# Performance work log

Hardware: AMD Instinct MI355X
Metric: run time of the kernel (lower is better)

The kernel has to match this reference:

```python
import jax, jax.numpy as jnp
import numpy as np

ALPHA = 0.2          # LeakyReLU negative slope
NEG_BIG = -9e15      # mask value from original code


def setup_inputs() -> dict:
    key = jax.random.key(0)
    k1, k2, k3, k4 = jax.random.split(key, 4)
    B, N, F_in, F_out = 16, 1024, 256, 256
    x = jax.random.normal(k1, (B, N, F_in), dtype=jnp.float32)
    adj = jax.random.randint(k2, (B, N, N), 0, 2, dtype=jnp.int32)
    # xavier-uniform-like scales
    W = jax.random.normal(k3, (F_in, F_out), dtype=jnp.float32) * np.sqrt(2.0 / (F_in + F_out))
    a = jax.random.normal(k4, (2 * F_out, 1), dtype=jnp.float32) * np.sqrt(2.0 / (2 * F_out + 1))
    return {"x": x, "adj": adj, "W": W, "a": a}


def reference(x, adj, W, a):
    # x: [B,N,Fin], adj: [B,N,N] (int mask), W: [Fin,Fout], a: [2*Fout,1]
    F_out = a.shape[0] // 2
    h = jnp.einsum("bni,io->bno", x, W)            # [B,N,Fout]
    # Decompose a into left/right halves: e_ij = lrelu(a_l.h_i + a_r.h_j)
    a_l = a[:F_out, 0]                               # [Fout]
    a_r = a[F_out:, 0]                               # [Fout]
    el = h @ a_l                                     # [B,N] score contribution of target i
    er = h @ a_r                                     # [B,N] score contribution of source j
    e = jax.nn.leaky_relu(el[:, :, None] + er[:, None, :], ALPHA)  # [B,N,N]
    e = jnp.where(adj > 0, e, NEG_BIG)
    attn = jax.nn.softmax(e, axis=-1)                # masked softmax over neighbors j
    # weighted sum of neighbor features; concat with n_heads=1 is identity
    return jnp.einsum("bij,bjo->bio", attn, h)       # [B,N,Fout]
```

## Files before the change

### kernel.cpp

```cpp
#include <hip/hip_runtime.h>
#include <stdint.h>

#define ALPHA 0.2f
#define NEG_BIG -9000000000000000.0f
#define L2E 1.4426950408889634f

typedef __attribute__((ext_vector_type(8))) short bf16x8;
typedef __attribute__((ext_vector_type(8))) unsigned short u16x8;
typedef __attribute__((ext_vector_type(4))) float f32x4;

__device__ __forceinline__ unsigned short f2bf(float f) {
    unsigned int u = __float_as_uint(f);
    u += 0x7fffu + ((u >> 16) & 1u);
    return (unsigned short)(u >> 16);
}

__device__ __forceinline__ void gload_lds16(const void* g, void* l) {
    __builtin_amdgcn_global_load_lds(
        (const __attribute__((address_space(1))) unsigned int*)g,
        (__attribute__((address_space(3))) unsigned int*)l, 16, 0, 0);
}

__global__ void wt_wa_kernel(const float* __restrict__ W,
                             const float* __restrict__ a,
                             unsigned short* __restrict__ Wtbf,
                             float* __restrict__ wa) {
    const int t = threadIdx.x;
    if (blockIdx.x < 256) {
        const int o = blockIdx.x;
        Wtbf[o * 256 + t] = f2bf(W[t * 256 + o]);
    } else {
        float sl = 0.f, sr = 0.f;
        const float* wr = W + t * 256;
        for (int o = 0; o < 256; ++o) {
            const float wv = wr[o];
            sl += wv * a[o];
            sr += wv * a[256 + o];
        }
        wa[t] = sl;
        wa[256 + t] = sr;
    }
}

__global__ __launch_bounds__(256) void eler2x_kernel(
    const float* __restrict__ x, const float* __restrict__ wa,
    float* __restrict__ el, float* __restrict__ er,
    unsigned short* __restrict__ xbf)
{
    const int w = threadIdx.x >> 6, l = threadIdx.x & 63;
    const int r = blockIdx.x * 4 + w;
    const float4 xv = *(const float4*)(x + (size_t)r * 256 + l * 4);
    const float4 al = *(const float4*)(wa + l * 4);
    const float4 ar = *(const float4*)(wa + 256 + l * 4);

    ushort4 xb;
    xb.x = f2bf(xv.x); xb.y = f2bf(xv.y); xb.z = f2bf(xv.z); xb.w = f2bf(xv.w);
    *(ushort4*)(xbf + (size_t)r * 256 + l * 4) = xb;

    float sl = xv.x * al.x + xv.y * al.y + xv.z * al.z + xv.w * al.w;
    float sr = xv.x * ar.x + xv.y * ar.y + xv.z * ar.z + xv.w * ar.w;
#pragma unroll
    for (int off = 32; off >= 1; off >>= 1) {
        sl += __shfl_xor(sl, off);
        sr += __shfl_xor(sr, off);
    }
    if (l == 0) { el[r] = sl * L2E; er[r] = sr * L2E; }
}

__global__ __launch_bounds__(256) void gemm_h(
    const unsigned short* __restrict__ A,
    const unsigned short* __restrict__ Bt,
    unsigned short* __restrict__ C)
{
    __shared__ __align__(16) unsigned short As[2 * 64 * 64];
    __shared__ __align__(16) unsigned short Bs[2 * 128 * 64];

    const int tid = threadIdx.x;
    const int w = tid >> 6, l = tid & 63;
    const int q = l >> 4, ml = l & 15;
    const int wm = (w >> 1) * 32;
    const int wn = (w & 1) * 64;
    const int m0 = blockIdx.y * 64;
    const int n0 = blockIdx.x * 128;

    f32x4 acc[2][4];
#pragma unroll
    for (int i = 0; i < 2; ++i)
#pragma unroll
        for (int j = 0; j < 4; ++j) {
            f32x4 z = {0.f, 0.f, 0.f, 0.f};
            acc[i][j] = z;
        }

#define GSTAGE(BI, K0) do {                                                   \
    _Pragma("unroll")                                                         \
    for (int c_ = 0; c_ < 2; ++c_) {                                          \
        const int cb_ = c_ * 256 + (w << 6);                                  \
        const int p_ = cb_ + l;                                               \
        const int r_ = p_ >> 3;                                               \
        const int cc_ = (p_ & 7) ^ (r_ & 7);                                  \
        gload_lds16(A + (size_t)(m0 + r_) * 256 + (K0) + cc_ * 8,             \
                    As + (BI) * 4096 + cb_ * 8);                              \
    }                                                                         \
    _Pragma("unroll")                                                         \
    for (int c_ = 0; c_ < 4; ++c_) {                                          \
        const int cb_ = c_ * 256 + (w << 6);                                  \
        const int p_ = cb_ + l;                                               \
        const int r_ = p_ >> 3;                                               \
        const int cc_ = (p_ & 7) ^ (r_ & 7);                                  \
        gload_lds16(Bt + (size_t)(n0 + r_) * 256 + (K0) + cc_ * 8,            \
                    Bs + (BI) * 8192 + cb_ * 8);                              \
    } } while (0)

    GSTAGE(0, 0);

    for (int s = 0; s < 4; ++s) {
        const int cur = s & 1;
        if (s + 1 < 4) {
            GSTAGE((s + 1) & 1, (s + 1) * 64);
            asm volatile("s_waitcnt vmcnt(6) lgkmcnt(0)" ::: "memory");
        } else {
            asm volatile("s_waitcnt vmcnt(0) lgkmcnt(0)" ::: "memory");
        }
        __builtin_amdgcn_s_barrier();
        __builtin_amdgcn_sched_barrier(0);

        const unsigned short* Ab = As + cur * 4096;
        const unsigned short* Bb = Bs + cur * 8192;
        bf16x8 aF[2][2], bF[2][4];
#pragma unroll
        for (int ks = 0; ks < 2; ++ks) {
#pragma unroll
            for (int mt = 0; mt < 2; ++mt) {
                const int mm = wm + mt * 16 + ml;
                aF[ks][mt] = *(const bf16x8*)(Ab + (mm * 8 + ((ks * 4 + q) ^ (mm & 7))) * 8);
            }
#pragma unroll
            for (int nt = 0; nt < 4; ++nt) {
                const int nn = wn + nt * 16 + ml;
                bF[ks][nt] = *(const bf16x8*)(Bb + (nn * 8 + ((ks * 4 + q) ^ (nn & 7))) * 8);
            }
        }
#pragma unroll
        for (int ks = 0; ks < 2; ++ks)
            for (int mt = 0; mt < 2; ++mt)
                for (int nt = 0; nt < 4; ++nt)
                    acc[mt][nt] = __builtin_amdgcn_mfma_f32_16x16x32_bf16(
                        aF[ks][mt], bF[ks][nt], acc[mt][nt], 0, 0, 0);

        asm volatile("s_waitcnt lgkmcnt(0)" ::: "memory");
        __builtin_amdgcn_s_barrier();
    }
#undef GSTAGE

    for (int mt = 0; mt < 2; ++mt)
        for (int nt = 0; nt < 4; ++nt) {
            const int gn = n0 + wn + nt * 16 + ml;
            for (int r = 0; r < 4; ++r) {
                const int gm = m0 + wm + mt * 16 + q * 4 + r;
                C[(size_t)gm * 16384 + gn] = f2bf(acc[mt][nt][r]);
            }
        }
}

__global__ __launch_bounds__(512) void maskpv_kernel(
    const int* __restrict__ adj,
    const float* __restrict__ el2,
    const float* __restrict__ er2,
    const unsigned short* __restrict__ hT,
    float* __restrict__ out)
{
    __shared__ float er_s[1024];
    __shared__ float s_s[32];
    __shared__ __align__(16) unsigned short Hs[2 * 256 * 64];
    __shared__ __align__(16) unsigned short Ps[2 * 32 * 72];

    const int tid = threadIdx.x;
    const int w = tid >> 6, l = tid & 63;
    const int q = l >> 4, ml = l & 15;
    const int wm = (w >> 2) * 16;
    const int wn = (w & 3) * 64;

    const int bid = blockIdx.x;
    const int slot = bid >> 3;
    const int b = ((bid & 7) << 1) | (slot >> 5);
    const int i0 = (slot & 31) * 32;

    const int ib = tid >> 4;
    const int js = (tid & 15) * 4;
    const int rg = (b << 10) + i0 + ib;
    const float el2i = el2[rg];

    const unsigned short* hb = hT + (size_t)b * 1024;

#define STAGE(BI, T) do {                                                     \
    const int jb_ = (T) * 64;                                                 \
    _Pragma("unroll")                                                         \
    for (int c_ = 0; c_ < 4; ++c_) {                                          \
        const int cb_ = c_ * 512 + tid;                                       \
        const int r_ = cb_ >> 3;                                              \
        const int cc_ = (cb_ & 7) ^ (r_ & 7);                                 \
        gload_lds16(hb + (size_t)r_ * 16384 + jb_ + cc_ * 8,                  \
                    Hs + (BI) * 16384 + (cb_ << 3));                          \
    } } while (0)

    STAGE(0, 0);

    *(float2*)(er_s + tid * 2) = *(const float2*)(er2 + (b << 10) + tid * 2);

    const int* arow = adj + (size_t)rg * 1024;
    unsigned mw0 = 0, mw1 = 0;
    {
        int4 av[8];
#pragma unroll
        for (int i = 0; i < 8; ++i)
            av[i] = *(const int4*)(arow + i * 64 + js);
#pragma unroll
        for (int i = 0; i < 8; ++i) {
            const unsigned bits =
                (av[i].x > 0 ? 1u : 0u) | (av[i].y > 0 ? 2u : 0u) |
                (av[i].z > 0 ? 4u : 0u) | (av[i].w > 0 ? 8u : 0u);
            mw0 |= bits << (i * 4);
        }
#pragma unroll
        for (int i = 0; i < 8; ++i)
            av[i] = *(const int4*)(arow + (i + 8) * 64 + js);
#pragma unroll
        for (int i = 0; i < 8; ++i) {
            const unsigned bits =
                (av[i].x > 0 ? 1u : 0u) | (av[i].y > 0 ? 2u : 0u) |
                (av[i].z > 0 ? 4u : 0u) | (av[i].w > 0 ? 8u : 0u);
            mw1 |= bits << (i * 4);
        }
    }

    asm volatile("s_waitcnt lgkmcnt(0)" ::: "memory");
    __builtin_amdgcn_s_barrier();

    f32x4 acc[4];
#pragma unroll
    for (int j = 0; j < 4; ++j) {
        f32x4 z = {0.f, 0.f, 0.f, 0.f};
        acc[j] = z;
    }
    float s0 = 0.f, s1 = 0.f, s2 = 0.f, s3 = 0.f;

#define BUILDR(BI, T) do {                                                    \
    const float4 ev_ = *(const float4*)(er_s + (T) * 64 + js);                \
    const unsigned mv_ =                                                      \
        (((T) < 8) ? (mw0 >> ((T) * 4)) : (mw1 >> (((T) - 8) * 4))) & 0xFu;   \
    float e0_ = el2i + ev_.x; e0_ = fmaxf(e0_, ALPHA * e0_);                  \
    float e1_ = el2i + ev_.y; e1_ = fmaxf(e1_, ALPHA * e1_);                  \
    float e2_ = el2i + ev_.z; e2_ = fmaxf(e2_, ALPHA * e2_);                  \
    float e3_ = el2i + ev_.w; e3_ = fmaxf(e3_, ALPHA * e3_);                  \
    ushort4 pv_;                                                              \
    pv_.x = (mv_ & 1u) ? f2bf(exp2f(e0_)) : (unsigned short)0;                \
    pv_.y = (mv_ & 2u) ? f2bf(exp2f(e1_)) : (unsigned short)0;                \
    pv_.z = (mv_ & 4u) ? f2bf(exp2f(e2_)) : (unsigned short)0;                \
    pv_.w = (mv_ & 8u) ? f2bf(exp2f(e3_)) : (unsigned short)0;                \
    s0 += __uint_as_float((unsigned)pv_.x << 16);                             \
    s1 += __uint_as_float((unsigned)pv_.y << 16);                             \
    s2 += __uint_as_float((unsigned)pv_.z << 16);                             \
    s3 += __uint_as_float((unsigned)pv_.w << 16);                             \
    *(ushort4*)(Ps + (BI) * 2304 + ib * 72 + js) = pv_;                       \
    } while (0)

#define COMPUTE(BI) do {                                                      \
    bf16x8 aF_[2], bF_[2][4];                                                 \
    _Pragma("unroll")                                                         \
    for (int ks_ = 0; ks_ < 2; ++ks_)                                         \
        aF_[ks_] = *(const bf16x8*)(Ps + (BI) * 2304 +                        \
                                    (wm + ml) * 72 + ks_ * 32 + q * 8);       \
    _Pragma("unroll")                                                         \
    for (int ks_ = 0; ks_ < 2; ++ks_)                                         \
        _Pragma("unroll")                                                     \
        for (int nt_ = 0; nt_ < 4; ++nt_) {                                   \
            const int oc_ = wn + nt_ * 16 + ml;                               \
            const int sl_ = (ks_ * 4 + q) ^ (oc_ & 7);                        \
            bF_[ks_][nt_] = *(const bf16x8*)(Hs + (BI) * 16384 +              \
                                             oc_ * 64 + sl_ * 8);             \
        }                                                                     \
    __builtin_amdgcn_s_setprio(1);                                            \
    _Pragma("unroll")                                                         \
    for (int ks_ = 0; ks_ < 2; ++ks_)                                         \
        _Pragma("unroll")                                                     \
        for (int nt_ = 0; nt_ < 4; ++nt_)                                     \
            acc[nt_] = __builtin_amdgcn_mfma_f32_16x16x32_bf16(               \
                aF_[ks_], bF_[ks_][nt_], acc[nt_], 0, 0, 0);                  \
    __builtin_amdgcn_s_setprio(0);                                            \
    } while (0)

#pragma unroll
    for (int t = 0; t < 16; ++t) {
        const int cur = t & 1;
        if (t + 1 < 16) STAGE((t + 1) & 1, t + 1);
        BUILDR(cur, t);
        if (t + 1 < 16)
            asm volatile("s_waitcnt vmcnt(4) lgkmcnt(0)" ::: "memory");
        else
            asm volatile("s_waitcnt vmcnt(0) lgkmcnt(0)" ::: "memory");
        __builtin_amdgcn_s_barrier();
        __builtin_amdgcn_sched_barrier(0);
        COMPUTE(cur);
        asm volatile("s_waitcnt lgkmcnt(0)" ::: "memory");
        __builtin_amdgcn_s_barrier();
    }

#undef STAGE
#undef BUILDR
#undef COMPUTE

    float ssum = (s0 + s1) + (s2 + s3);
#pragma unroll
    for (int off = 1; off <= 8; off <<= 1) ssum += __shfl_xor(ssum, off);
    if ((tid & 15) == 0) s_s[ib] = ssum;
    __syncthreads();

    float* ob = out + (size_t)b * 262144;
    float rinv[4];
#pragma unroll
    for (int r = 0; r < 4; ++r) rinv[r] = 1.0f / s_s[wm + q * 4 + r];
#pragma unroll
    for (int nt = 0; nt < 4; ++nt) {
        const int gn = wn + nt * 16 + ml;
#pragma unroll
        for (int r = 0; r < 4; ++r) {
            const int gm = i0 + wm + q * 4 + r;
            ob[(size_t)gm * 256 + gn] = acc[nt][r] * rinv[r];
        }
    }
}

extern "C" void kernel_launch(void* const* d_in, const int* in_sizes, int n_in,
                              void* d_out, int out_size, void* d_ws, size_t ws_size,
                              hipStream_t stream) {
    const float* x   = (const float*)d_in[0];
    const int*   adj = (const int*)d_in[1];
    const float* W   = (const float*)d_in[2];
    const float* a   = (const float*)d_in[3];
    float* out = (float*)d_out;

    char* ws = (char*)d_ws;
    unsigned short* Wtbf  = (unsigned short*)(ws);
    float* wa             = (float*)(ws + 131072);
    unsigned short* xbf   = (unsigned short*)(ws + 133120);
    unsigned short* h_T   = (unsigned short*)(ws + 8521728);
    float* el             = (float*)(ws + 16910336);
    float* er             = (float*)(ws + 16975872);

    wt_wa_kernel<<<dim3(257), dim3(256), 0, stream>>>(W, a, Wtbf, wa);

    eler2x_kernel<<<dim3(4096), dim3(256), 0, stream>>>(x, wa, el, er, xbf);

    gemm_h<<<dim3(128, 4), dim3(256), 0, stream>>>(Wtbf, xbf, h_T);

    maskpv_kernel<<<dim3(512), dim3(512), 0, stream>>>(adj, el, er, h_T, out);
}
```

Measured before the change: 159.8 us.

## Load H operands directly into registers instead of staging through LDS

The maskpv kernel no longer stages hT tiles into shared memory with global_load_lds. Each wave now loads its B fragments straight from global memory into registers, double-buffered across two register sets, and the loop is restructured into a two-step pipeline that alternates building P with MFMA compute. Launch bounds now request 4 blocks per CU. This removes the LDS footprint for H and the LDS read traffic, allowing higher occupancy. In exchange, the global loads are less coalesced (16 bytes per lane at 32 KB row strides), there is more register pressure, and the barrier count per step goes up.

```diff
diff --git a/kernel.cpp b/kernel.cpp
--- a/kernel.cpp
+++ b/kernel.cpp
@@ -2,11 +2,9 @@
 #include <stdint.h>
 
 #define ALPHA 0.2f
-#define NEG_BIG -9000000000000000.0f
 #define L2E 1.4426950408889634f
 
 typedef __attribute__((ext_vector_type(8))) short bf16x8;
-typedef __attribute__((ext_vector_type(8))) unsigned short u16x8;
 typedef __attribute__((ext_vector_type(4))) float f32x4;
 
 __device__ __forceinline__ unsigned short f2bf(float f) {
@@ -19,6 +17,11 @@
     __builtin_amdgcn_global_load_lds(
         (const __attribute__((address_space(1))) unsigned int*)g,
         (__attribute__((address_space(3))) unsigned int*)l, 16, 0, 0);
+}
+
+__device__ __forceinline__ void bar_lds() {
+    asm volatile("s_waitcnt lgkmcnt(0)" ::: "memory");
+    __builtin_amdgcn_s_barrier();
 }
 
 __global__ void wt_wa_kernel(const float* __restrict__ W,
@@ -163,7 +166,7 @@
         }
 }
 
-__global__ __launch_bounds__(512) void maskpv_kernel(
+__global__ __launch_bounds__(512, 4) void maskpv_kernel(
     const int* __restrict__ adj,
     const float* __restrict__ el2,
     const float* __restrict__ er2,
@@ -172,7 +175,6 @@
 {
     __shared__ float er_s[1024];
     __shared__ float s_s[32];
-    __shared__ __align__(16) unsigned short Hs[2 * 256 * 64];
     __shared__ __align__(16) unsigned short Ps[2 * 32 * 72];
 
     const int tid = threadIdx.x;
@@ -193,18 +195,21 @@
 
     const unsigned short* hb = hT + (size_t)b * 1024;
 
-#define STAGE(BI, T) do {                                                     \
-    const int jb_ = (T) * 64;                                                 \
-    _Pragma("unroll")                                                         \
-    for (int c_ = 0; c_ < 4; ++c_) {                                          \
-        const int cb_ = c_ * 512 + tid;                                       \
-        const int r_ = cb_ >> 3;                                              \
-        const int cc_ = (cb_ & 7) ^ (r_ & 7);                                 \
-        gload_lds16(hb + (size_t)r_ * 16384 + jb_ + cc_ * 8,                  \
-                    Hs + (BI) * 16384 + (cb_ << 3));                          \
+    const unsigned short* bp[4];
+#pragma unroll
+    for (int nt = 0; nt < 4; ++nt)
+        bp[nt] = hb + (size_t)(wn + nt * 16 + ml) * 16384 + q * 8;
+
+    bf16x8 BA[8], BB[8];
+
+#define LOADB(B, T) do {                                                      \
+    _Pragma("unroll")                                                         \
+    for (int nt_ = 0; nt_ < 4; ++nt_) {                                       \
+        B[nt_]     = *(const bf16x8*)(bp[nt_] + (T) * 64);                    \
+        B[4 + nt_] = *(const bf16x8*)(bp[nt_] + (T) * 64 + 32);               \
     } } while (0)
 
-    STAGE(0, 0);
+    LOADB(BA, 0);
 
     *(float2*)(er_s + tid * 2) = *(const float2*)(er2 + (b << 10) + tid * 2);
 
@@ -234,8 +239,7 @@
         }
     }
 
-    asm volatile("s_waitcnt lgkmcnt(0)" ::: "memory");
-    __builtin_amdgcn_s_barrier();
+    bar_lds();
 
     f32x4 acc[4];
 #pragma unroll
@@ -245,7 +249,7 @@
     }
     float s0 = 0.f, s1 = 0.f, s2 = 0.f, s3 = 0.f;
 
-#define BUILDR(BI, T) do {                                                    \
+#define BUILDP(BI, T) do {                                                    \
     const float4 ev_ = *(const float4*)(er_s + (T) * 64 + js);                \
     const unsigned mv_ =                                                      \
         (((T) < 8) ? (mw0 >> ((T) * 4)) : (mw1 >> (((T) - 8) * 4))) & 0xFu;   \
@@ -265,49 +269,41 @@
     *(ushort4*)(Ps + (BI) * 2304 + ib * 72 + js) = pv_;                       \
     } while (0)
 
-#define COMPUTE(BI) do {                                                      \
-    bf16x8 aF_[2], bF_[2][4];                                                 \
+#define COMPUTE(BI, B) do {                                                   \
+    bf16x8 aF_[2];                                                            \
     _Pragma("unroll")                                                         \
     for (int ks_ = 0; ks_ < 2; ++ks_)                                         \
         aF_[ks_] = *(const bf16x8*)(Ps + (BI) * 2304 +                        \
                                     (wm + ml) * 72 + ks_ * 32 + q * 8);       \
-    _Pragma("unroll")                                                         \
-    for (int ks_ = 0; ks_ < 2; ++ks_)                                         \
-        _Pragma("unroll")                                                     \
-        for (int nt_ = 0; nt_ < 4; ++nt_) {                                   \
-            const int oc_ = wn + nt_ * 16 + ml;                               \
-            const int sl_ = (ks_ * 4 + q) ^ (oc_ & 7);                        \
-            bF_[ks_][nt_] = *(const bf16x8*)(Hs + (BI) * 16384 +              \
-                                             oc_ * 64 + sl_ * 8);             \
-        }                                                                     \
     __builtin_amdgcn_s_setprio(1);                                            \
     _Pragma("unroll")                                                         \
     for (int ks_ = 0; ks_ < 2; ++ks_)                                         \
         _Pragma("unroll")                                                     \
         for (int nt_ = 0; nt_ < 4; ++nt_)                                     \
             acc[nt_] = __builtin_amdgcn_mfma_f32_16x16x32_bf16(               \
-                aF_[ks_], bF_[ks_][nt_], acc[nt_], 0, 0, 0);                  \
+                aF_[ks_], B[ks_ * 4 + nt_], acc[nt_], 0, 0, 0);               \
     __builtin_amdgcn_s_setprio(0);                                            \
     } while (0)
 
-#pragma unroll
-    for (int t = 0; t < 16; ++t) {
-        const int cur = t & 1;
-        if (t + 1 < 16) STAGE((t + 1) & 1, t + 1);
-        BUILDR(cur, t);
-        if (t + 1 < 16)
-            asm volatile("s_waitcnt vmcnt(4) lgkmcnt(0)" ::: "memory");
-        else
-            asm volatile("s_waitcnt vmcnt(0) lgkmcnt(0)" ::: "memory");
-        __builtin_amdgcn_s_barrier();
-        __builtin_amdgcn_sched_barrier(0);
-        COMPUTE(cur);
-        asm volatile("s_waitcnt lgkmcnt(0)" ::: "memory");
-        __builtin_amdgcn_s_barrier();
-    }
-
-#undef STAGE
-#undef BUILDR
+    BUILDP(0, 0);
+
+    for (int t = 0; t < 16; t += 2) {
+        LOADB(BB, t + 1);
+        BUILDP(1, t + 1);
+        bar_lds();
+        COMPUTE(0, BA);
+        bar_lds();
+        if (t + 2 < 16) {
+            LOADB(BA, t + 2);
+            BUILDP(0, t + 2);
+        }
+        bar_lds();
+        COMPUTE(1, BB);
+        bar_lds();
+    }
+
+#undef LOADB
+#undef BUILDP
 #undef COMPUTE
 
     float ssum = (s0 + s1) + (s2 + s3);
```

Result: slower. 216.8 us (+35.6%).

## Split masked attention-PV kernel across output-column halves with smaller j tiles

Applied to the files above, without the earlier changes.

The attention/PV kernel now launches 1024 blocks of 256 threads, each covering 32 rows and half of the 256 output features, instead of 512 blocks of 512 threads covering all features. The j dimension is processed in 32-wide steps instead of 64, with smaller LDS buffers and a matching swizzle, which raises block count and occupancy. The cost is that each output half recomputes the exp/mask probabilities and rereads the adjacency rows, doubling adj traffic (the largest input), and the loop has more barriers per unit of work.

```diff
diff --git a/kernel.cpp b/kernel.cpp
--- a/kernel.cpp
+++ b/kernel.cpp
@@ -2,11 +2,9 @@
 #include <stdint.h>
 
 #define ALPHA 0.2f
-#define NEG_BIG -9000000000000000.0f
 #define L2E 1.4426950408889634f
 
 typedef __attribute__((ext_vector_type(8))) short bf16x8;
-typedef __attribute__((ext_vector_type(8))) unsigned short u16x8;
 typedef __attribute__((ext_vector_type(4))) float f32x4;
 
 __device__ __forceinline__ unsigned short f2bf(float f) {
@@ -163,7 +161,7 @@
         }
 }
 
-__global__ __launch_bounds__(512) void maskpv_kernel(
+__global__ __launch_bounds__(256) void maskpv_kernel(
     const int* __restrict__ adj,
     const float* __restrict__ el2,
     const float* __restrict__ er2,
@@ -172,66 +170,61 @@
 {
     __shared__ float er_s[1024];
     __shared__ float s_s[32];
-    __shared__ __align__(16) unsigned short Hs[2 * 256 * 64];
-    __shared__ __align__(16) unsigned short Ps[2 * 32 * 72];
+    __shared__ __align__(16) unsigned short Hs[2 * 128 * 32];
+    __shared__ __align__(16) unsigned short Ps[2 * 32 * 40];
 
     const int tid = threadIdx.x;
     const int w = tid >> 6, l = tid & 63;
     const int q = l >> 4, ml = l & 15;
-    const int wm = (w >> 2) * 16;
-    const int wn = (w & 3) * 64;
+    const int wm = (w >> 1) * 16;
+    const int wn = (w & 1) * 64;
 
     const int bid = blockIdx.x;
     const int slot = bid >> 3;
-    const int b = ((bid & 7) << 1) | (slot >> 5);
-    const int i0 = (slot & 31) * 32;
-
-    const int ib = tid >> 4;
-    const int js = (tid & 15) * 4;
+    const int b = ((bid & 7) << 1) | (slot >> 6);
+    const int rem = slot & 63;
+    const int i0 = (rem >> 1) * 32;
+    const int oh = rem & 1;
+
+    const int ib = tid >> 3;
+    const int js = (tid & 7) * 4;
     const int rg = (b << 10) + i0 + ib;
     const float el2i = el2[rg];
 
-    const unsigned short* hb = hT + (size_t)b * 1024;
+    const unsigned short* hb = hT + (size_t)b * 1024 + (size_t)oh * 128 * 16384;
 
 #define STAGE(BI, T) do {                                                     \
-    const int jb_ = (T) * 64;                                                 \
-    _Pragma("unroll")                                                         \
-    for (int c_ = 0; c_ < 4; ++c_) {                                          \
-        const int cb_ = c_ * 512 + tid;                                       \
-        const int r_ = cb_ >> 3;                                              \
-        const int cc_ = (cb_ & 7) ^ (r_ & 7);                                 \
+    const int jb_ = (T) * 32;                                                 \
+    _Pragma("unroll")                                                         \
+    for (int c_ = 0; c_ < 2; ++c_) {                                          \
+        const int cb_ = c_ * 256 + tid;                                       \
+        const int r_ = cb_ >> 2;                                              \
+        const int cc_ = (cb_ & 3) ^ ((r_ >> 1) & 3);                          \
         gload_lds16(hb + (size_t)r_ * 16384 + jb_ + cc_ * 8,                  \
-                    Hs + (BI) * 16384 + (cb_ << 3));                          \
+                    Hs + (BI) * 4096 + (cb_ << 3));                           \
     } } while (0)
 
     STAGE(0, 0);
 
-    *(float2*)(er_s + tid * 2) = *(const float2*)(er2 + (b << 10) + tid * 2);
-
-    const int* arow = adj + (size_t)rg * 1024;
-    unsigned mw0 = 0, mw1 = 0;
-    {
+    *(float4*)(er_s + tid * 4) = *(const float4*)(er2 + (b << 10) + tid * 4);
+
+    const int* arow = adj + (size_t)rg * 1024 + js;
+    unsigned mw[4] = {0u, 0u, 0u, 0u};
+#pragma unroll
+    for (int bt = 0; bt < 4; ++bt) {
         int4 av[8];
 #pragma unroll
         for (int i = 0; i < 8; ++i)
-            av[i] = *(const int4*)(arow + i * 64 + js);
+            av[i] = *(const int4*)(arow + (bt * 8 + i) * 32);
+        unsigned acc_bits = 0;
 #pragma unroll
         for (int i = 0; i < 8; ++i) {
             const unsigned bits =
                 (av[i].x > 0 ? 1u : 0u) | (av[i].y > 0 ? 2u : 0u) |
                 (av[i].z > 0 ? 4u : 0u) | (av[i].w > 0 ? 8u : 0u);
-            mw0 |= bits << (i * 4);
-        }
-#pragma unroll
-        for (int i = 0; i < 8; ++i)
-            av[i] = *(const int4*)(arow + (i + 8) * 64 + js);
-#pragma unroll
-        for (int i = 0; i < 8; ++i) {
-            const unsigned bits =
-                (av[i].x > 0 ? 1u : 0u) | (av[i].y > 0 ? 2u : 0u) |
-                (av[i].z > 0 ? 4u : 0u) | (av[i].w > 0 ? 8u : 0u);
-            mw1 |= bits << (i * 4);
-        }
+            acc_bits |= bits << (i * 4);
+        }
+        mw[bt] = acc_bits;
     }
 
     asm volatile("s_waitcnt lgkmcnt(0)" ::: "memory");
@@ -246,9 +239,8 @@
     float s0 = 0.f, s1 = 0.f, s2 = 0.f, s3 = 0.f;
 
 #define BUILDR(BI, T) do {                                                    \
-    const float4 ev_ = *(const float4*)(er_s + (T) * 64 + js);                \
-    const unsigned mv_ =                                                      \
-        (((T) < 8) ? (mw0 >> ((T) * 4)) : (mw1 >> (((T) - 8) * 4))) & 0xFu;   \
+    const float4 ev_ = *(const float4*)(er_s + (T) * 32 + js);                \
+    const unsigned mv_ = (mw[(T) >> 3] >> (((T) & 7) * 4)) & 0xFu;            \
     float e0_ = el2i + ev_.x; e0_ = fmaxf(e0_, ALPHA * e0_);                  \
     float e1_ = el2i + ev_.y; e1_ = fmaxf(e1_, ALPHA * e1_);                  \
     float e2_ = el2i + ev_.z; e2_ = fmaxf(e2_, ALPHA * e2_);                  \
@@ -262,41 +254,34 @@
     s1 += __uint_as_float((unsigned)pv_.y << 16);                             \
     s2 += __uint_as_float((unsigned)pv_.z << 16);                             \
     s3 += __uint_as_float((unsigned)pv_.w << 16);                             \
-    *(ushort4*)(Ps + (BI) * 2304 + ib * 72 + js) = pv_;                       \
+    *(ushort4*)(Ps + (BI) * 1280 + ib * 40 + js) = pv_;                       \
     } while (0)
 
 #define COMPUTE(BI) do {                                                      \
-    bf16x8 aF_[2], bF_[2][4];                                                 \
-    _Pragma("unroll")                                                         \
-    for (int ks_ = 0; ks_ < 2; ++ks_)                                         \
-        aF_[ks_] = *(const bf16x8*)(Ps + (BI) * 2304 +                        \
-                                    (wm + ml) * 72 + ks_ * 32 + q * 8);       \
-    _Pragma("unroll")                                                         \
-    for (int ks_ = 0; ks_ < 2; ++ks_)                                         \
-        _Pragma("unroll")                                                     \
-        for (int nt_ = 0; nt_ < 4; ++nt_) {                                   \
-            const int oc_ = wn + nt_ * 16 + ml;                               \
-            const int sl_ = (ks_ * 4 + q) ^ (oc_ & 7);                        \
-            bF_[ks_][nt_] = *(const bf16x8*)(Hs + (BI) * 16384 +              \
-                                             oc_ * 64 + sl_ * 8);             \
-        }                                                                     \
+    const bf16x8 aF_ = *(const bf16x8*)(Ps + (BI) * 1280 +                    \
+                                        (wm + ml) * 40 + q * 8);              \
+    bf16x8 bF_[4];                                                            \
+    _Pragma("unroll")                                                         \
+    for (int nt_ = 0; nt_ < 4; ++nt_) {                                       \
+        const int oc_ = wn + nt_ * 16 + ml;                                   \
+        const int sl_ = q ^ ((oc_ >> 1) & 3);                                 \
+        bF_[nt_] = *(const bf16x8*)(Hs + (BI) * 4096 + oc_ * 32 + sl_ * 8);   \
+    }                                                                         \
     __builtin_amdgcn_s_setprio(1);                                            \
     _Pragma("unroll")                                                         \
-    for (int ks_ = 0; ks_ < 2; ++ks_)                                         \
-        _Pragma("unroll")                                                     \
-        for (int nt_ = 0; nt_ < 4; ++nt_)                                     \
-            acc[nt_] = __builtin_amdgcn_mfma_f32_16x16x32_bf16(               \
-                aF_[ks_], bF_[ks_][nt_], acc[nt_], 0, 0, 0);                  \
+    for (int nt_ = 0; nt_ < 4; ++nt_)                                         \
+        acc[nt_] = __builtin_amdgcn_mfma_f32_16x16x32_bf16(                   \
+            aF_, bF_[nt_], acc[nt_], 0, 0, 0);                                \
     __builtin_amdgcn_s_setprio(0);                                            \
     } while (0)
 
 #pragma unroll
-    for (int t = 0; t < 16; ++t) {
+    for (int t = 0; t < 32; ++t) {
         const int cur = t & 1;
-        if (t + 1 < 16) STAGE((t + 1) & 1, t + 1);
+        if (t + 1 < 32) STAGE((t + 1) & 1, t + 1);
         BUILDR(cur, t);
-        if (t + 1 < 16)
-            asm volatile("s_waitcnt vmcnt(4) lgkmcnt(0)" ::: "memory");
+        if (t + 1 < 32)
+            asm volatile("s_waitcnt vmcnt(2) lgkmcnt(0)" ::: "memory");
         else
             asm volatile("s_waitcnt vmcnt(0) lgkmcnt(0)" ::: "memory");
         __builtin_amdgcn_s_barrier();
@@ -312,11 +297,11 @@
 
     float ssum = (s0 + s1) + (s2 + s3);
 #pragma unroll
-    for (int off = 1; off <= 8; off <<= 1) ssum += __shfl_xor(ssum, off);
-    if ((tid & 15) == 0) s_s[ib] = ssum;
+    for (int off = 1; off <= 4; off <<= 1) ssum += __shfl_xor(ssum, off);
+    if ((tid & 7) == 0) s_s[ib] = ssum;
     __syncthreads();
 
-    float* ob = out + (size_t)b * 262144;
+    float* ob = out + (size_t)b * 262144 + oh * 128;
     float rinv[4];
 #pragma unroll
     for (int r = 0; r < 4; ++r) rinv[r] = 1.0f / s_s[wm + q * 4 + r];
@@ -354,5 +339,5 @@
 
     gemm_h<<<dim3(128, 4), dim3(256), 0, stream>>>(Wtbf, xbf, h_T);
 
-    maskpv_kernel<<<dim3(512), dim3(512), 0, stream>>>(adj, el, er, h_T, out);
-}
+    maskpv_kernel<<<dim3(1024), dim3(256), 0, stream>>>(adj, el, er, h_T, out);
+}
```

New measurement: 170.7 us. 1.07x slower.

## Deepen H staging pipeline to four half-tile buffers with prefetch ahead

Applied to the files above, without the earlier changes.

Splits the H tile staging into four 32-column buffers instead of two 64-column ones, so loads run two half-tiles further ahead of use. Prefetches for the next iterations are issued after each compute barrier rather than before the score build. The aim is to hide more global-to-LDS latency behind the softmax-score and MFMA work while keeping the same LDS footprint. The swizzle pattern changes to match the narrower rows. The vmcnt(4) wait count is unchanged even though more loads are now outstanding, which may make the waits less precise and adds a risk around synchronization.

```diff
diff --git a/kernel.cpp b/kernel.cpp
--- a/kernel.cpp
+++ b/kernel.cpp
@@ -2,11 +2,9 @@
 #include <stdint.h>
 
 #define ALPHA 0.2f
-#define NEG_BIG -9000000000000000.0f
 #define L2E 1.4426950408889634f
 
 typedef __attribute__((ext_vector_type(8))) short bf16x8;
-typedef __attribute__((ext_vector_type(8))) unsigned short u16x8;
 typedef __attribute__((ext_vector_type(4))) float f32x4;
 
 __device__ __forceinline__ unsigned short f2bf(float f) {
@@ -172,7 +170,7 @@
 {
     __shared__ float er_s[1024];
     __shared__ float s_s[32];
-    __shared__ __align__(16) unsigned short Hs[2 * 256 * 64];
+    __shared__ __align__(16) unsigned short Hs[4 * 256 * 32];
     __shared__ __align__(16) unsigned short Ps[2 * 32 * 72];
 
     const int tid = threadIdx.x;
@@ -193,18 +191,18 @@
 
     const unsigned short* hb = hT + (size_t)b * 1024;
 
-#define STAGE(BI, T) do {                                                     \
-    const int jb_ = (T) * 64;                                                 \
-    _Pragma("unroll")                                                         \
-    for (int c_ = 0; c_ < 4; ++c_) {                                          \
+#define STAGE(S, T) do {                                                      \
+    const int jb_ = (T) * 32;                                                 \
+    _Pragma("unroll")                                                         \
+    for (int c_ = 0; c_ < 2; ++c_) {                                          \
         const int cb_ = c_ * 512 + tid;                                       \
-        const int r_ = cb_ >> 3;                                              \
-        const int cc_ = (cb_ & 7) ^ (r_ & 7);                                 \
+        const int r_ = cb_ >> 2;                                              \
+        const int cc_ = (cb_ & 3) ^ ((r_ >> 1) & 3);                          \
         gload_lds16(hb + (size_t)r_ * 16384 + jb_ + cc_ * 8,                  \
-                    Hs + (BI) * 16384 + (cb_ << 3));                          \
+                    Hs + (S) * 8192 + (cb_ << 3));                            \
     } } while (0)
 
-    STAGE(0, 0);
+    STAGE(0, 0); STAGE(1, 1); STAGE(2, 2); STAGE(3, 3);
 
     *(float2*)(er_s + tid * 2) = *(const float2*)(er2 + (b << 10) + tid * 2);
 
@@ -265,21 +263,22 @@
     *(ushort4*)(Ps + (BI) * 2304 + ib * 72 + js) = pv_;                       \
     } while (0)
 
-#define COMPUTE(BI) do {                                                      \
+#define COMPUTE(BI, T) do {                                                   \
     bf16x8 aF_[2], bF_[2][4];                                                 \
     _Pragma("unroll")                                                         \
     for (int ks_ = 0; ks_ < 2; ++ks_)                                         \
         aF_[ks_] = *(const bf16x8*)(Ps + (BI) * 2304 +                        \
                                     (wm + ml) * 72 + ks_ * 32 + q * 8);       \
     _Pragma("unroll")                                                         \
-    for (int ks_ = 0; ks_ < 2; ++ks_)                                         \
+    for (int ks_ = 0; ks_ < 2; ++ks_) {                                       \
+        const int sb_ = ((2 * (T) + ks_) & 3) * 8192;                         \
         _Pragma("unroll")                                                     \
         for (int nt_ = 0; nt_ < 4; ++nt_) {                                   \
             const int oc_ = wn + nt_ * 16 + ml;                               \
-            const int sl_ = (ks_ * 4 + q) ^ (oc_ & 7);                        \
-            bF_[ks_][nt_] = *(const bf16x8*)(Hs + (BI) * 16384 +              \
-                                             oc_ * 64 + sl_ * 8);             \
+            const int sl_ = q ^ ((oc_ >> 1) & 3);                             \
+            bF_[ks_][nt_] = *(const bf16x8*)(Hs + sb_ + oc_ * 32 + sl_ * 8);  \
         }                                                                     \
+    }                                                                         \
     __builtin_amdgcn_s_setprio(1);                                            \
     _Pragma("unroll")                                                         \
     for (int ks_ = 0; ks_ < 2; ++ks_)                                         \
@@ -292,18 +291,20 @@
 
 #pragma unroll
     for (int t = 0; t < 16; ++t) {
-        const int cur = t & 1;
-        if (t + 1 < 16) STAGE((t + 1) & 1, t + 1);
-        BUILDR(cur, t);
-        if (t + 1 < 16)
+        BUILDR(t & 1, t);
+        if (t < 15)
             asm volatile("s_waitcnt vmcnt(4) lgkmcnt(0)" ::: "memory");
         else
             asm volatile("s_waitcnt vmcnt(0) lgkmcnt(0)" ::: "memory");
         __builtin_amdgcn_s_barrier();
         __builtin_amdgcn_sched_barrier(0);
-        COMPUTE(cur);
+        COMPUTE(t & 1, t);
         asm volatile("s_waitcnt lgkmcnt(0)" ::: "memory");
         __builtin_amdgcn_s_barrier();
+        if (t <= 13) {
+            STAGE((2 * t + 4) & 3, 2 * t + 4);
+            STAGE((2 * t + 5) & 3, 2 * t + 5);
+        }
     }
 
 #undef STAGE
```

Result: no change. 159.9 us (+0.1%).
